# Kernel optimization log

Hardware: AMD Instinct MI355X
Metric: run time of the kernel (lower is better)

## Reference

```python
import jax, jax.numpy as jnp
import numpy as np

B, L, DIMS, HEADS, HD = 4, 2048, 1024, 16, 64
EPS = 1e-5

def swish(x):
    return x * jax.nn.sigmoid(x)

def layer_norm(x):
    mu = jnp.mean(x, axis=-1, keepdims=True)
    var = jnp.var(x, axis=-1, keepdims=True)
    return (x - mu) / jnp.sqrt(var + EPS)

def setup_inputs() -> dict:
    key = jax.random.key(0)
    k1, k2, k3 = jax.random.split(key, 3)
    x = jax.random.normal(k1, (B, L, DIMS), dtype=jnp.float32)
    W_fc = jax.random.normal(k2, (DIMS, HEADS * HD * 3), dtype=jnp.float32) * 0.02
    b_fc = jnp.zeros((HEADS * HD * 3,), dtype=jnp.float32)
    W_out = jax.random.normal(k3, (HD * HEADS, DIMS), dtype=jnp.float32) * 0.02
    b_out = jnp.zeros((DIMS,), dtype=jnp.float32)
    return {"x": x, "W_fc": W_fc, "b_fc": b_fc, "W_out": W_out, "b_out": b_out}

def reference(x, W_fc, b_fc, W_out, b_out):
    # dropout p=0.3 is identity at inference
    qkv = swish(x @ W_fc + b_fc)                       # [B,L,H*3*hd]
    qkv = qkv.reshape(B, L, HEADS, 3 * HD)
    q, k, v = jnp.split(qkv, 3, axis=-1)                # each [B,L,H,hd]
    # NOTE: no 1/sqrt(hd) scaling, matching the source
    att = jax.nn.softmax(jnp.einsum('bwhd,bmhd->bhwm', q, k), axis=-1)
    new_v = jnp.einsum('bhwm,bmhd->bwhd', att, v).reshape(B, L, HEADS * HD)
    m = swish(new_v @ W_out + b_out)                   # [B,L,dims]
    return layer_norm(m + x)
```

## Files before the change

kernel.cpp:

```cpp
#include <hip/hip_runtime.h>
#include <hip/hip_bf16.h>
#include <stdint.h>

typedef float  f32x4  __attribute__((ext_vector_type(4)));
typedef short  bf16x8 __attribute__((ext_vector_type(8)));

__device__ __forceinline__ unsigned short f2bf(float f) {
  union { __hip_bfloat16 b; unsigned short u; } cv;
  cv.b = __float2bfloat16(f);
  return cv.u;
}

template <int CTRL>
__device__ __forceinline__ float dpp_mv(float x) {
  int v = __builtin_bit_cast(int, x);
  v = __builtin_amdgcn_update_dpp(v, v, CTRL, 0xF, 0xF, false);
  return __builtin_bit_cast(float, v);
}
__device__ __forceinline__ float rowmax16(float x) {
  x = fmaxf(x, dpp_mv<0x121>(x));
  x = fmaxf(x, dpp_mv<0x122>(x));
  x = fmaxf(x, dpp_mv<0x124>(x));
  x = fmaxf(x, dpp_mv<0x128>(x));
  return x;
}
__device__ __forceinline__ float rowsum16(float x) {
  x += dpp_mv<0x121>(x);
  x += dpp_mv<0x122>(x);
  x += dpp_mv<0x124>(x);
  x += dpp_mv<0x128>(x);
  return x;
}

__global__ __launch_bounds__(256) void k_cvt_bf16(const float* __restrict__ in,
                                                  __hip_bfloat16* __restrict__ out) {
  size_t i = (size_t)blockIdx.x * 256 + threadIdx.x;
  float4 a = *(const float4*)(in + i * 8);
  float4 b = *(const float4*)(in + i * 8 + 4);
  bf16x8 o;
  o[0] = (short)f2bf(a.x); o[1] = (short)f2bf(a.y);
  o[2] = (short)f2bf(a.z); o[3] = (short)f2bf(a.w);
  o[4] = (short)f2bf(b.x); o[5] = (short)f2bf(b.y);
  o[6] = (short)f2bf(b.z); o[7] = (short)f2bf(b.w);
  *(bf16x8*)(out + i * 8) = o;
}

__global__ __launch_bounds__(256) void k_transpose_bf16(const float* __restrict__ in,
                                                        __hip_bfloat16* __restrict__ out,
                                                        int K, int N) {
  __shared__ float tile[32][33];
  int t = threadIdx.x;
  int k0 = blockIdx.y * 32, n0 = blockIdx.x * 32;
  {
    int kl = t >> 3, nl = (t & 7) * 4;
    float4 v = *(const float4*)(in + (size_t)(k0 + kl) * N + n0 + nl);
    tile[kl][nl] = v.x; tile[kl][nl + 1] = v.y; tile[kl][nl + 2] = v.z; tile[kl][nl + 3] = v.w;
  }
  __syncthreads();
  {
    int nl = t >> 3, kl = (t & 7) * 4;
    union { short4 s; unsigned short u[4]; } o;
    #pragma unroll
    for (int i = 0; i < 4; ++i) o.u[i] = f2bf(tile[kl + i][nl]);
    *(short4*)(out + (size_t)(n0 + nl) * K + k0 + kl) = o.s;
  }
}

__device__ __forceinline__ void stage128x32(const __hip_bfloat16* gsrc_row0, int ld_elem,
                                            char* lds_tile, int t) {
  int w = t >> 6, lam = t & 63;
  #pragma unroll
  for (int i = 0; i < 2; ++i) {
    int idx = w * 1024 + i * 4096 + lam * 16;
    int row = idx >> 6;
    int cph = (idx >> 4) & 3;
    int csrc = cph ^ ((row >> 1) & 3);
    const char* src = (const char*)(gsrc_row0 + (size_t)row * ld_elem) + csrc * 16;
    __builtin_amdgcn_global_load_lds(
        (const __attribute__((address_space(1))) uint32_t*)src,
        (__attribute__((address_space(3))) uint32_t*)(lds_tile + w * 1024 + i * 4096),
        16, 0, 0);
  }
}

__device__ __forceinline__ bf16x8 frag64(const char* tile, int row, int chunk) {
  int c = chunk ^ ((row >> 1) & 3);
  return *(const bf16x8*)(tile + row * 64 + c * 16);
}

__global__ __launch_bounds__(256) void k_gemm_fc(const __hip_bfloat16* __restrict__ A,
                                                 const __hip_bfloat16* __restrict__ Bt,
                                                 const float* __restrict__ bias,
                                                 __hip_bfloat16* __restrict__ C,
                                                 int M, int N, int K) {
  __shared__ char lds[16384];
  char* As = lds; char* Bs = lds + 8192;
  const int t = threadIdx.x, l = t & 63, w = t >> 6;
  const int bm0 = blockIdx.y * 128, bn0 = blockIdx.x * 128;
  const int wm = (w >> 1) * 64, wn = (w & 1) * 64;
  f32x4 acc[4][4] = {};
  for (int kt = 0; kt < K; kt += 32) {
    stage128x32(A + (size_t)bm0 * K + kt, K, As, t);
    stage128x32(Bt + (size_t)bn0 * K + kt, K, Bs, t);
    __syncthreads();
    bf16x8 af[4], bfr[4];
    #pragma unroll
    for (int mi = 0; mi < 4; ++mi) af[mi] = frag64(As, wm + mi * 16 + (l & 15), l >> 4);
    #pragma unroll
    for (int ni = 0; ni < 4; ++ni) bfr[ni] = frag64(Bs, wn + ni * 16 + (l & 15), l >> 4);
    #pragma unroll
    for (int mi = 0; mi < 4; ++mi)
      #pragma unroll
      for (int ni = 0; ni < 4; ++ni)
        acc[mi][ni] = __builtin_amdgcn_mfma_f32_16x16x32_bf16(af[mi], bfr[ni], acc[mi][ni], 0, 0, 0);
    __syncthreads();
  }
  #pragma unroll
  for (int mi = 0; mi < 4; ++mi)
    #pragma unroll
    for (int ni = 0; ni < 4; ++ni)
      #pragma unroll
      for (int r = 0; r < 4; ++r) {
        int row = bm0 + wm + mi * 16 + (l >> 4) * 4 + r;
        int col = bn0 + wn + ni * 16 + (l & 15);
        float v = acc[mi][ni][r] + bias[col];
        v = v / (1.0f + __expf(-v));
        *(unsigned short*)((char*)C + ((size_t)row * N + col) * 2) = f2bf(v);
      }
}

__global__ __launch_bounds__(256) void k_gemm_out(const __hip_bfloat16* __restrict__ A,
                                                  const __hip_bfloat16* __restrict__ Bt,
                                                  const float* __restrict__ bias,
                                                  const float* __restrict__ X,
                                                  float* __restrict__ C,
                                                  int M, int N, int K) {
  __shared__ char lds[16384];
  char* As = lds; char* Bs = lds + 8192;
  const int t = threadIdx.x, l = t & 63, w = t >> 6;
  const int bm0 = blockIdx.y * 128, bn0 = blockIdx.x * 128;
  const int wm = (w >> 1) * 64, wn = (w & 1) * 64;
  f32x4 acc[4][4] = {};
  for (int kt = 0; kt < K; kt += 32) {
    stage128x32(A + (size_t)bm0 * K + kt, K, As, t);
    stage128x32(Bt + (size_t)bn0 * K + kt, K, Bs, t);
    __syncthreads();
    bf16x8 af[4], bfr[4];
    #pragma unroll
    for (int mi = 0; mi < 4; ++mi) af[mi] = frag64(As, wm + mi * 16 + (l & 15), l >> 4);
    #pragma unroll
    for (int ni = 0; ni < 4; ++ni) bfr[ni] = frag64(Bs, wn + ni * 16 + (l & 15), l >> 4);
    #pragma unroll
    for (int mi = 0; mi < 4; ++mi)
      #pragma unroll
      for (int ni = 0; ni < 4; ++ni)
        acc[mi][ni] = __builtin_amdgcn_mfma_f32_16x16x32_bf16(af[mi], bfr[ni], acc[mi][ni], 0, 0, 0);
    __syncthreads();
  }
  #pragma unroll
  for (int mi = 0; mi < 4; ++mi)
    #pragma unroll
    for (int ni = 0; ni < 4; ++ni)
      #pragma unroll
      for (int r = 0; r < 4; ++r) {
        int row = bm0 + wm + mi * 16 + (l >> 4) * 4 + r;
        int col = bn0 + wn + ni * 16 + (l & 15);
        float v = acc[mi][ni][r] + bias[col];
        v = v / (1.0f + __expf(-v));
        v += X[(size_t)row * N + col];
        C[(size_t)row * N + col] = v;
      }
}

__global__ __launch_bounds__(256) void k_attn(const __hip_bfloat16* __restrict__ qkv,
                                              __hip_bfloat16* __restrict__ nv) {
  __shared__ char lds[40960];
  const int t = threadIdx.x, l = t & 63, w = t >> 6;
  char* Ps = lds + 24576 + w * 4096;
  const int b = blockIdx.z, h = blockIdx.y;
  const int q0 = blockIdx.x * 128 + w * 32;
  const size_t seq0 = (size_t)b * 2048;
  const float LOG2E = 1.4426950408889634f;

  bf16x8 qf[2][2];
  #pragma unroll
  for (int mi = 0; mi < 2; ++mi)
    #pragma unroll
    for (int ks = 0; ks < 2; ++ks) {
      int row = q0 + mi * 16 + (l & 15);
      int col = ks * 32 + 8 * (l >> 4);
      bf16x8 raw = *(const bf16x8*)(qkv + (seq0 + row) * 3072 + h * 192 + col);
      #pragma unroll
      for (int j = 0; j < 8; ++j) {
        unsigned int u = ((unsigned int)(unsigned short)raw[j]) << 16;
        float f = __builtin_bit_cast(float, u) * LOG2E;
        qf[mi][ks][j] = (short)f2bf(f);
      }
    }

  auto k_issue = [&](int kv0, char* Kd) {
    #pragma unroll
    for (int i = 0; i < 2; ++i) {
      int row = i * 32 + w * 8 + (l >> 3);
      int cl = (l & 7) ^ (l >> 3);
      const char* src = (const char*)(qkv + (seq0 + kv0 + row) * 3072 + h * 192 + 64 + cl * 8);
      __builtin_amdgcn_global_load_lds(
          (const __attribute__((address_space(1))) uint32_t*)src,
          (__attribute__((address_space(3))) uint32_t*)(Kd + w * 1024 + i * 4096),
          16, 0, 0);
    }
  };
  const int vkv = t & 63, vdg = t >> 6;
  const int vp = 4 * (vkv & 15) + (vkv >> 4);
  const int vwithin = (2 * vp) & 15;
  const int vchunk = vp >> 3;
  union { uint4 q[2]; unsigned short s[16]; } vreg;
  auto v_issue = [&](int kv0) {
    const __hip_bfloat16* src = qkv + (seq0 + kv0 + vkv) * 3072 + h * 192 + 128 + vdg * 16;
    vreg.q[0] = *(const uint4*)(src);
    vreg.q[1] = *(const uint4*)(src + 8);
  };
  auto v_write = [&](char* Vd) {
    #pragma unroll
    for (int j = 0; j < 16; ++j) {
      int d = vdg * 16 + j;
      *(unsigned short*)(Vd + d * 128 + ((vchunk ^ (d & 7)) << 4) + vwithin) = vreg.s[j];
    }
  };

  f32x4 O[2][4] = {};
  float m_run[2][4], lp[2][4];
  #pragma unroll
  for (int mi = 0; mi < 2; ++mi)
    #pragma unroll
    for (int r = 0; r < 4; ++r) { m_run[mi][r] = -1e30f; lp[mi][r] = 0.0f; }

  k_issue(0, lds);
  v_issue(0);
  v_write(lds + 16384);
  __syncthreads();

  for (int tIdx = 0; tIdx < 32; ++tIdx) {
    const int cur = tIdx & 1, nxt = cur ^ 1;
    const char* Kc = lds + cur * 8192;
    const char* Vc = lds + 16384;
    if (tIdx < 31) {
      k_issue((tIdx + 1) * 64, lds + nxt * 8192);
      v_issue((tIdx + 1) * 64);
    }

    f32x4 S[2][4] = {};
    __builtin_amdgcn_s_setprio(1);
    #pragma unroll
    for (int ni = 0; ni < 4; ++ni) {
      int kvr = ni * 16 + (l & 15);
      #pragma unroll
      for (int ks = 0; ks < 2; ++ks) {
        bf16x8 kf = *(const bf16x8*)(Kc + kvr * 128 + (((ks * 4 + (l >> 4)) ^ (kvr & 7)) << 4));
        #pragma unroll
        for (int mi = 0; mi < 2; ++mi)
          S[mi][ni] = __builtin_amdgcn_mfma_f32_16x16x32_bf16(qf[mi][ks], kf, S[mi][ni], 0, 0, 0);
      }
    }
    __builtin_amdgcn_s_setprio(0);

    float tm[2][4];
    bool ok = true;
    #pragma unroll
    for (int mi = 0; mi < 2; ++mi)
      #pragma unroll
      for (int r = 0; r < 4; ++r) {
        float a = fmaxf(fmaxf(S[mi][0][r], S[mi][1][r]), fmaxf(S[mi][2][r], S[mi][3][r]));
        tm[mi][r] = a;
        ok = ok && (a <= m_run[mi][r] + 11.0f);
      }
    const int c = l & 15;
    if (__all(ok)) {
      #pragma unroll
      for (int mi = 0; mi < 2; ++mi)
        #pragma unroll
        for (int r = 0; r < 4; ++r) {
          float mn = m_run[mi][r];
          float p0 = __builtin_amdgcn_exp2f(S[mi][0][r] - mn);
          float p1 = __builtin_amdgcn_exp2f(S[mi][1][r] - mn);
          float p2 = __builtin_amdgcn_exp2f(S[mi][2][r] - mn);
          float p3 = __builtin_amdgcn_exp2f(S[mi][3][r] - mn);
          lp[mi][r] += (p0 + p1) + (p2 + p3);
          uint32_t d0, d1;
          asm("v_cvt_pk_bf16_f32 %0, %1, %2" : "=v"(d0) : "v"(p0), "v"(p1));
          asm("v_cvt_pk_bf16_f32 %0, %1, %2" : "=v"(d1) : "v"(p2), "v"(p3));
          uint2 pk; pk.x = d0; pk.y = d1;
          int q = mi * 16 + (l >> 4) * 4 + r;
          *(uint2*)(Ps + q * 128 + ((((c >> 1) ^ (q & 7))) << 4) + ((c & 1) << 3)) = pk;
        }
    } else {
      #pragma unroll
      for (int mi = 0; mi < 2; ++mi)
        #pragma unroll
        for (int r = 0; r < 4; ++r) {
          float mo = m_run[mi][r];
          float mn = fmaxf(mo, rowmax16(tm[mi][r]));
          float sc = __builtin_amdgcn_exp2f(mo - mn);
          m_run[mi][r] = mn;
          float p0 = __builtin_amdgcn_exp2f(S[mi][0][r] - mn);
          float p1 = __builtin_amdgcn_exp2f(S[mi][1][r] - mn);
          float p2 = __builtin_amdgcn_exp2f(S[mi][2][r] - mn);
          float p3 = __builtin_amdgcn_exp2f(S[mi][3][r] - mn);
          lp[mi][r] = lp[mi][r] * sc + (p0 + p1) + (p2 + p3);
          O[mi][0][r] *= sc; O[mi][1][r] *= sc; O[mi][2][r] *= sc; O[mi][3][r] *= sc;
          uint32_t d0, d1;
          asm("v_cvt_pk_bf16_f32 %0, %1, %2" : "=v"(d0) : "v"(p0), "v"(p1));
          asm("v_cvt_pk_bf16_f32 %0, %1, %2" : "=v"(d1) : "v"(p2), "v"(p3));
          uint2 pk; pk.x = d0; pk.y = d1;
          int q = mi * 16 + (l >> 4) * 4 + r;
          *(uint2*)(Ps + q * 128 + ((((c >> 1) ^ (q & 7))) << 4) + ((c & 1) << 3)) = pk;
        }
    }

    bf16x8 pa[2][2];
    #pragma unroll
    for (int mi = 0; mi < 2; ++mi) {
      int q = mi * 16 + (l & 15);
      #pragma unroll
      for (int ks = 0; ks < 2; ++ks)
        pa[mi][ks] = *(const bf16x8*)(Ps + q * 128 + (((ks * 4 + (l >> 4)) ^ (q & 7)) << 4));
    }
    __builtin_amdgcn_s_setprio(1);
    #pragma unroll
    for (int ni = 0; ni < 4; ++ni) {
      int dv = ni * 16 + (l & 15);
      #pragma unroll
      for (int ks = 0; ks < 2; ++ks) {
        bf16x8 vf = *(const bf16x8*)(Vc + dv * 128 + (((ks * 4 + (l >> 4)) ^ (dv & 7)) << 4));
        #pragma unroll
        for (int mi = 0; mi < 2; ++mi)
          O[mi][ni] = __builtin_amdgcn_mfma_f32_16x16x32_bf16(pa[mi][ks], vf, O[mi][ni], 0, 0, 0);
      }
    }
    __builtin_amdgcn_s_setprio(0);

    __syncthreads();
    if (tIdx < 31) v_write(lds + 16384);
    __syncthreads();
  }

  #pragma unroll
  for (int mi = 0; mi < 2; ++mi) {
    #pragma unroll
    for (int r = 0; r < 4; ++r) {
      float inv = 1.0f / rowsum16(lp[mi][r]);
      int row = q0 + mi * 16 + (l >> 4) * 4 + r;
      #pragma unroll
      for (int ni = 0; ni < 4; ++ni) {
        int col = h * 64 + ni * 16 + (l & 15);
        *(unsigned short*)((char*)nv + (((seq0 + row) * 1024 + col)) * 2) =
            f2bf(O[mi][ni][r] * inv);
      }
    }
  }
}

__global__ __launch_bounds__(256) void k_ln(float* __restrict__ io) {
  int row = blockIdx.x, t = threadIdx.x;
  float* p = io + (size_t)row * 1024;
  float4 v = *(const float4*)(p + t * 4);
  float s = v.x + v.y + v.z + v.w;
  float q = v.x * v.x + v.y * v.y + v.z * v.z + v.w * v.w;
  #pragma unroll
  for (int off = 32; off > 0; off >>= 1) { s += __shfl_xor(s, off); q += __shfl_xor(q, off); }
  __shared__ float red[8];
  if ((t & 63) == 0) { red[t >> 6] = s; red[4 + (t >> 6)] = q; }
  __syncthreads();
  s = red[0] + red[1] + red[2] + red[3];
  q = red[4] + red[5] + red[6] + red[7];
  float mu = s * (1.0f / 1024.0f);
  float var = q * (1.0f / 1024.0f) - mu * mu;
  float rs = rsqrtf(var + 1e-5f);
  float4 o;
  o.x = (v.x - mu) * rs; o.y = (v.y - mu) * rs; o.z = (v.z - mu) * rs; o.w = (v.w - mu) * rs;
  *(float4*)(p + t * 4) = o;
}

extern "C" void kernel_launch(void* const* d_in, const int* in_sizes, int n_in,
                              void* d_out, int out_size, void* d_ws, size_t ws_size,
                              hipStream_t stream) {
  const float* x    = (const float*)d_in[0];
  const float* Wfc  = (const float*)d_in[1];
  const float* bfc  = (const float*)d_in[2];
  const float* Wout = (const float*)d_in[3];
  const float* bout = (const float*)d_in[4];
  float* out = (float*)d_out;

  char* ws = (char*)d_ws;
  __hip_bfloat16* xb   = (__hip_bfloat16*)(ws);
  __hip_bfloat16* wfct = (__hip_bfloat16*)(ws + 16777216);
  __hip_bfloat16* wot  = (__hip_bfloat16*)(ws + 23068672);
  __hip_bfloat16* qkvb = (__hip_bfloat16*)(ws + 25165824);
  __hip_bfloat16* nvb  = (__hip_bfloat16*)(ws + 75497472);

  k_cvt_bf16<<<4096, 256, 0, stream>>>(x, xb);
  k_transpose_bf16<<<dim3(96, 32), 256, 0, stream>>>(Wfc, wfct, 1024, 3072);
  k_transpose_bf16<<<dim3(32, 32), 256, 0, stream>>>(Wout, wot, 1024, 1024);
  k_gemm_fc<<<dim3(24, 64), 256, 0, stream>>>(xb, wfct, bfc, qkvb, 8192, 3072, 1024);
  k_attn<<<dim3(16, 16, 4), 256, 0, stream>>>(qkvb, nvb);
  k_gemm_out<<<dim3(8, 64), 256, 0, stream>>>(nvb, wot, bout, x, out, 8192, 1024, 1024);
  k_ln<<<8192, 256, 0, stream>>>(out);
}
```

Measured before the change: 273.2 us.

## Process two 64-row KV sub-blocks per barrier round in attention kernel

```diff
diff --git a/kernel.cpp b/kernel.cpp
--- a/kernel.cpp
+++ b/kernel.cpp
@@ -174,9 +174,9 @@
 
 __global__ __launch_bounds__(256) void k_attn(const __hip_bfloat16* __restrict__ qkv,
                                               __hip_bfloat16* __restrict__ nv) {
-  __shared__ char lds[40960];
+  __shared__ char lds[65536];
   const int t = threadIdx.x, l = t & 63, w = t >> 6;
-  char* Ps = lds + 24576 + w * 4096;
+  char* Ps = lds + 49152 + w * 4096;
   const int b = blockIdx.z, h = blockIdx.y;
   const int q0 = blockIdx.x * 128 + w * 32;
   const size_t seq0 = (size_t)b * 2048;
@@ -200,7 +200,7 @@
 
   auto k_issue = [&](int kv0, char* Kd) {
     #pragma unroll
-    for (int i = 0; i < 2; ++i) {
+    for (int i = 0; i < 4; ++i) {
       int row = i * 32 + w * 8 + (l >> 3);
       int cl = (l & 7) ^ (l >> 3);
       const char* src = (const char*)(qkv + (seq0 + kv0 + row) * 3072 + h * 192 + 64 + cl * 8);
@@ -214,18 +214,25 @@
   const int vp = 4 * (vkv & 15) + (vkv >> 4);
   const int vwithin = (2 * vp) & 15;
   const int vchunk = vp >> 3;
-  union { uint4 q[2]; unsigned short s[16]; } vreg;
+  union { uint4 q[4]; unsigned short s[32]; } vreg;
   auto v_issue = [&](int kv0) {
-    const __hip_bfloat16* src = qkv + (seq0 + kv0 + vkv) * 3072 + h * 192 + 128 + vdg * 16;
-    vreg.q[0] = *(const uint4*)(src);
-    vreg.q[1] = *(const uint4*)(src + 8);
+    #pragma unroll
+    for (int sb = 0; sb < 2; ++sb) {
+      const __hip_bfloat16* src =
+          qkv + (seq0 + kv0 + sb * 64 + vkv) * 3072 + h * 192 + 128 + vdg * 16;
+      vreg.q[sb * 2]     = *(const uint4*)(src);
+      vreg.q[sb * 2 + 1] = *(const uint4*)(src + 8);
+    }
   };
   auto v_write = [&](char* Vd) {
     #pragma unroll
-    for (int j = 0; j < 16; ++j) {
-      int d = vdg * 16 + j;
-      *(unsigned short*)(Vd + d * 128 + ((vchunk ^ (d & 7)) << 4) + vwithin) = vreg.s[j];
-    }
+    for (int sb = 0; sb < 2; ++sb)
+      #pragma unroll
+      for (int j = 0; j < 16; ++j) {
+        int d = vdg * 16 + j;
+        *(unsigned short*)(Vd + sb * 8192 + d * 128 + ((vchunk ^ (d & 7)) << 4) + vwithin) =
+            vreg.s[sb * 16 + j];
+      }
   };
 
   f32x4 O[2][4] = {};
@@ -237,110 +244,116 @@
 
   k_issue(0, lds);
   v_issue(0);
-  v_write(lds + 16384);
+  v_write(lds + 32768);
   __syncthreads();
 
-  for (int tIdx = 0; tIdx < 32; ++tIdx) {
-    const int cur = tIdx & 1, nxt = cur ^ 1;
-    const char* Kc = lds + cur * 8192;
-    const char* Vc = lds + 16384;
-    if (tIdx < 31) {
-      k_issue((tIdx + 1) * 64, lds + nxt * 8192);
-      v_issue((tIdx + 1) * 64);
-    }
-
-    f32x4 S[2][4] = {};
-    __builtin_amdgcn_s_setprio(1);
-    #pragma unroll
-    for (int ni = 0; ni < 4; ++ni) {
-      int kvr = ni * 16 + (l & 15);
-      #pragma unroll
-      for (int ks = 0; ks < 2; ++ks) {
-        bf16x8 kf = *(const bf16x8*)(Kc + kvr * 128 + (((ks * 4 + (l >> 4)) ^ (kvr & 7)) << 4));
+  for (int g = 0; g < 16; ++g) {
+    const int cur = g & 1, nxt = cur ^ 1;
+    const char* Kg = lds + cur * 16384;
+    const char* Vg = lds + 32768;
+    if (g < 15) {
+      k_issue((g + 1) * 128, lds + nxt * 16384);
+      v_issue((g + 1) * 128);
+    }
+
+    #pragma unroll
+    for (int sb = 0; sb < 2; ++sb) {
+      const char* Kc = Kg + sb * 8192;
+      const char* Vc = Vg + sb * 8192;
+
+      f32x4 S[2][4] = {};
+      __builtin_amdgcn_s_setprio(1);
+      #pragma unroll
+      for (int ni = 0; ni < 4; ++ni) {
+        int kvr = ni * 16 + (l & 15);
+        #pragma unroll
+        for (int ks = 0; ks < 2; ++ks) {
+          bf16x8 kf = *(const bf16x8*)(Kc + kvr * 128 + (((ks * 4 + (l >> 4)) ^ (kvr & 7)) << 4));
+          #pragma unroll
+          for (int mi = 0; mi < 2; ++mi)
+            S[mi][ni] = __builtin_amdgcn_mfma_f32_16x16x32_bf16(qf[mi][ks], kf, S[mi][ni], 0, 0, 0);
+        }
+      }
+      __builtin_amdgcn_s_setprio(0);
+
+      float tm[2][4];
+      bool ok = true;
+      #pragma unroll
+      for (int mi = 0; mi < 2; ++mi)
+        #pragma unroll
+        for (int r = 0; r < 4; ++r) {
+          float a = fmaxf(fmaxf(S[mi][0][r], S[mi][1][r]), fmaxf(S[mi][2][r], S[mi][3][r]));
+          tm[mi][r] = a;
+          ok = ok && (a <= m_run[mi][r] + 11.0f);
+        }
+      const int c = l & 15;
+      if (__all(ok)) {
         #pragma unroll
         for (int mi = 0; mi < 2; ++mi)
-          S[mi][ni] = __builtin_amdgcn_mfma_f32_16x16x32_bf16(qf[mi][ks], kf, S[mi][ni], 0, 0, 0);
-      }
-    }
-    __builtin_amdgcn_s_setprio(0);
-
-    float tm[2][4];
-    bool ok = true;
-    #pragma unroll
-    for (int mi = 0; mi < 2; ++mi)
-      #pragma unroll
-      for (int r = 0; r < 4; ++r) {
-        float a = fmaxf(fmaxf(S[mi][0][r], S[mi][1][r]), fmaxf(S[mi][2][r], S[mi][3][r]));
-        tm[mi][r] = a;
-        ok = ok && (a <= m_run[mi][r] + 11.0f);
-      }
-    const int c = l & 15;
-    if (__all(ok)) {
-      #pragma unroll
-      for (int mi = 0; mi < 2; ++mi)
-        #pragma unroll
-        for (int r = 0; r < 4; ++r) {
-          float mn = m_run[mi][r];
-          float p0 = __builtin_amdgcn_exp2f(S[mi][0][r] - mn);
-          float p1 = __builtin_amdgcn_exp2f(S[mi][1][r] - mn);
-          float p2 = __builtin_amdgcn_exp2f(S[mi][2][r] - mn);
-          float p3 = __builtin_amdgcn_exp2f(S[mi][3][r] - mn);
-          lp[mi][r] += (p0 + p1) + (p2 + p3);
-          uint32_t d0, d1;
-          asm("v_cvt_pk_bf16_f32 %0, %1, %2" : "=v"(d0) : "v"(p0), "v"(p1));
-          asm("v_cvt_pk_bf16_f32 %0, %1, %2" : "=v"(d1) : "v"(p2), "v"(p3));
-          uint2 pk; pk.x = d0; pk.y = d1;
-          int q = mi * 16 + (l >> 4) * 4 + r;
-          *(uint2*)(Ps + q * 128 + ((((c >> 1) ^ (q & 7))) << 4) + ((c & 1) << 3)) = pk;
+          #pragma unroll
+          for (int r = 0; r < 4; ++r) {
+            float mn = m_run[mi][r];
+            float p0 = __builtin_amdgcn_exp2f(S[mi][0][r] - mn);
+            float p1 = __builtin_amdgcn_exp2f(S[mi][1][r] - mn);
+            float p2 = __builtin_amdgcn_exp2f(S[mi][2][r] - mn);
+            float p3 = __builtin_amdgcn_exp2f(S[mi][3][r] - mn);
+            lp[mi][r] += (p0 + p1) + (p2 + p3);
+            uint32_t d0, d1;
+            asm("v_cvt_pk_bf16_f32 %0, %1, %2" : "=v"(d0) : "v"(p0), "v"(p1));
+            asm("v_cvt_pk_bf16_f32 %0, %1, %2" : "=v"(d1) : "v"(p2), "v"(p3));
+            uint2 pk; pk.x = d0; pk.y = d1;
+            int q = mi * 16 + (l >> 4) * 4 + r;
+            *(uint2*)(Ps + q * 128 + ((((c >> 1) ^ (q & 7))) << 4) + ((c & 1) << 3)) = pk;
+          }
+      } else {
+        #pragma unroll
+        for (int mi = 0; mi < 2; ++mi)
+          #pragma unroll
+          for (int r = 0; r < 4; ++r) {
+            float mo = m_run[mi][r];
+            float mn = fmaxf(mo, rowmax16(tm[mi][r]));
+            float sc = __builtin_amdgcn_exp2f(mo - mn);
+            m_run[mi][r] = mn;
+            float p0 = __builtin_amdgcn_exp2f(S[mi][0][r] - mn);
+            float p1 = __builtin_amdgcn_exp2f(S[mi][1][r] - mn);
+            float p2 = __builtin_amdgcn_exp2f(S[mi][2][r] - mn);
+            float p3 = __builtin_amdgcn_exp2f(S[mi][3][r] - mn);
+            lp[mi][r] = lp[mi][r] * sc + (p0 + p1) + (p2 + p3);
+            O[mi][0][r] *= sc; O[mi][1][r] *= sc; O[mi][2][r] *= sc; O[mi][3][r] *= sc;
+            uint32_t d0, d1;
+            asm("v_cvt_pk_bf16_f32 %0, %1, %2" : "=v"(d0) : "v"(p0), "v"(p1));
+            asm("v_cvt_pk_bf16_f32 %0, %1, %2" : "=v"(d1) : "v"(p2), "v"(p3));
+            uint2 pk; pk.x = d0; pk.y = d1;
+            int q = mi * 16 + (l >> 4) * 4 + r;
+            *(uint2*)(Ps + q * 128 + ((((c >> 1) ^ (q & 7))) << 4) + ((c & 1) << 3)) = pk;
+          }
+      }
+
+      bf16x8 pa[2][2];
+      #pragma unroll
+      for (int mi = 0; mi < 2; ++mi) {
+        int q = mi * 16 + (l & 15);
+        #pragma unroll
+        for (int ks = 0; ks < 2; ++ks)
+          pa[mi][ks] = *(const bf16x8*)(Ps + q * 128 + (((ks * 4 + (l >> 4)) ^ (q & 7)) << 4));
+      }
+      __builtin_amdgcn_s_setprio(1);
+      #pragma unroll
+      for (int ni = 0; ni < 4; ++ni) {
+        int dv = ni * 16 + (l & 15);
+        #pragma unroll
+        for (int ks = 0; ks < 2; ++ks) {
+          bf16x8 vf = *(const bf16x8*)(Vc + dv * 128 + (((ks * 4 + (l >> 4)) ^ (dv & 7)) << 4));
+          #pragma unroll
+          for (int mi = 0; mi < 2; ++mi)
+            O[mi][ni] = __builtin_amdgcn_mfma_f32_16x16x32_bf16(pa[mi][ks], vf, O[mi][ni], 0, 0, 0);
         }
-    } else {
-      #pragma unroll
-      for (int mi = 0; mi < 2; ++mi)
-        #pragma unroll
-        for (int r = 0; r < 4; ++r) {
-          float mo = m_run[mi][r];
-          float mn = fmaxf(mo, rowmax16(tm[mi][r]));
-          float sc = __builtin_amdgcn_exp2f(mo - mn);
-          m_run[mi][r] = mn;
-          float p0 = __builtin_amdgcn_exp2f(S[mi][0][r] - mn);
-          float p1 = __builtin_amdgcn_exp2f(S[mi][1][r] - mn);
-          float p2 = __builtin_amdgcn_exp2f(S[mi][2][r] - mn);
-          float p3 = __builtin_amdgcn_exp2f(S[mi][3][r] - mn);
-          lp[mi][r] = lp[mi][r] * sc + (p0 + p1) + (p2 + p3);
-          O[mi][0][r] *= sc; O[mi][1][r] *= sc; O[mi][2][r] *= sc; O[mi][3][r] *= sc;
-          uint32_t d0, d1;
-          asm("v_cvt_pk_bf16_f32 %0, %1, %2" : "=v"(d0) : "v"(p0), "v"(p1));
-          asm("v_cvt_pk_bf16_f32 %0, %1, %2" : "=v"(d1) : "v"(p2), "v"(p3));
-          uint2 pk; pk.x = d0; pk.y = d1;
-          int q = mi * 16 + (l >> 4) * 4 + r;
-          *(uint2*)(Ps + q * 128 + ((((c >> 1) ^ (q & 7))) << 4) + ((c & 1) << 3)) = pk;
-        }
-    }
-
-    bf16x8 pa[2][2];
-    #pragma unroll
-    for (int mi = 0; mi < 2; ++mi) {
-      int q = mi * 16 + (l & 15);
-      #pragma unroll
-      for (int ks = 0; ks < 2; ++ks)
-        pa[mi][ks] = *(const bf16x8*)(Ps + q * 128 + (((ks * 4 + (l >> 4)) ^ (q & 7)) << 4));
-    }
-    __builtin_amdgcn_s_setprio(1);
-    #pragma unroll
-    for (int ni = 0; ni < 4; ++ni) {
-      int dv = ni * 16 + (l & 15);
-      #pragma unroll
-      for (int ks = 0; ks < 2; ++ks) {
-        bf16x8 vf = *(const bf16x8*)(Vc + dv * 128 + (((ks * 4 + (l >> 4)) ^ (dv & 7)) << 4));
-        #pragma unroll
-        for (int mi = 0; mi < 2; ++mi)
-          O[mi][ni] = __builtin_amdgcn_mfma_f32_16x16x32_bf16(pa[mi][ks], vf, O[mi][ni], 0, 0, 0);
-      }
-    }
-    __builtin_amdgcn_s_setprio(0);
-
-    __syncthreads();
-    if (tIdx < 31) v_write(lds + 16384);
+      }
+      __builtin_amdgcn_s_setprio(0);
+    }
+
+    __syncthreads();
+    if (g < 15) v_write(lds + 32768);
     __syncthreads();
   }
 
```

Result: slower. 375.9 us (+37.6%).
